# Optimization experiments

Hardware: AMD Instinct MI355X
Metric: run time of the kernel (lower is better)

## Reference

```python
import jax, jax.numpy as jnp
import numpy as np
from jax import lax

EPS = 1e-5      # BatchNorm eps
SLOPE = 0.01    # LeakyReLU negative slope
SHIFT = 0.5     # ShiftedLeakyReLU downward shift (assumed)

# sign with clipped straight-through estimator (hardtanh STE)
@jax.custom_vjp
def binarize(x):
    return jnp.sign(x)

def _bin_fwd(x):
    return jnp.sign(x), x

def _bin_bwd(res, g):
    x = res
    return (g * (jnp.abs(x) <= 1.0).astype(g.dtype),)

binarize.defvjp(_bin_fwd, _bin_bwd)


def conv2d(x, w, b, stride, padding, groups):
    # x: [B,Cin,H,W], w: [Cout,Cin//groups,kh,kw]
    y = lax.conv_general_dilated(
        x, w,
        window_strides=(stride, stride),
        padding=[(padding, padding), (padding, padding)],
        dimension_numbers=('NCHW', 'OIHW', 'NCHW'),
        feature_group_count=groups,
    )
    return y + b[None, :, None, None]


def batchnorm(x, gamma, beta):
    # training-mode BN: batch statistics over (N,H,W)
    mean = jnp.mean(x, axis=(0, 2, 3), keepdims=True)
    var = jnp.var(x, axis=(0, 2, 3), keepdims=True)
    xn = (x - mean) * lax.rsqrt(var + EPS)
    return xn * gamma[None, :, None, None] + beta[None, :, None, None]


def shifted_leaky_relu(x):
    return jax.nn.leaky_relu(x, SLOPE) - SHIFT


def block(x, w, b, gamma, beta, stride, padding, groups, binarize_w):
    wq = binarize(w) if binarize_w else w
    x = conv2d(x, wq, b, stride, padding, groups)
    x = batchnorm(x, gamma, beta)
    x = shifted_leaky_relu(x)
    return binarize(x)


def setup_inputs() -> dict:
    D, B, C, NCLS = 10000, 16, 1, 10
    key = jax.random.key(0)
    ks = jax.random.split(key, 6)
    u = lambda k, shape: jax.random.uniform(k, shape, jnp.float32, -1.0, 1.0)
    return {
        "x":  jax.random.normal(ks[0], (B, C, 28, 28), jnp.float32),
        "W1": u(ks[1], (D, C, 5, 5)),  "b1": jnp.zeros((D,), jnp.float32),
        "g1": jnp.ones((D,), jnp.float32), "be1": jnp.zeros((D,), jnp.float32),
        "W2": u(ks[2], (D, 1, 3, 3)),  "b2": jnp.zeros((D,), jnp.float32),
        "g2": jnp.ones((D,), jnp.float32), "be2": jnp.zeros((D,), jnp.float32),
        "W3": u(ks[3], (D, 1, 6, 6)) * 0.1, "b3": jnp.zeros((D,), jnp.float32),
        "g3": jnp.ones((D,), jnp.float32), "be3": jnp.zeros((D,), jnp.float32),
        "Wc": u(ks[4], (NCLS, D)),
    }


def reference(x, W1, b1, g1, be1, W2, b2, g2, be2, W3, b3, g3, be3, Wc):
    D = Wc.shape[1]
    # encoder: binary conv -> BN -> shifted leaky relu -> binarize
    h = block(x, W1, b1, g1, be1, stride=2, padding=1, groups=1, binarize_w=True)   # [B,D,13,13]
    h = block(h, W2, b2, g2, be2, stride=2, padding=0, groups=D, binarize_w=True)   # [B,D,6,6]
    # final prototype conv (plain fp32 weights, depthwise, collapses spatial dims)
    h = block(h, W3, b3, g3, be3, stride=1, padding=0, groups=D, binarize_w=False)  # [B,D,1,1]
    h = h.reshape(h.shape[0], -1)                                                   # [B,D]
    # centroid similarity with sign-binarized class hypervectors
    sims = h @ binarize(Wc).T                                                       # [B,n_classes]
    return sims / jnp.sqrt(jnp.float32(D))
```

## Files before the change

kernel.cpp:

```cpp
#include <hip/hip_runtime.h>
#include <stdint.h>

__device__ __forceinline__ float sgnf(float v) {
    return (v > 0.f) ? 1.f : ((v < 0.f) ? -1.f : 0.f);
}

__global__ void prep_w1(const float* __restrict__ W1, float* __restrict__ w1q) {
    const int i = blockIdx.x * 256 + threadIdx.x;
    if (i < 250000) w1q[i] = sgnf(W1[i]);
}

__global__ __launch_bounds__(256, 2) void hdc_fused(
    const float* __restrict__ x,  const float* __restrict__ w1q,
    const float* __restrict__ b1, const float* __restrict__ g1,
    const float* __restrict__ be1,
    const float* __restrict__ W2, const float* __restrict__ b2,
    const float* __restrict__ g2, const float* __restrict__ be2,
    const float* __restrict__ W3, const float* __restrict__ b3,
    const float* __restrict__ g3, const float* __restrict__ be3,
    const float* __restrict__ Wc, const float* __restrict__ zrow,
    float* __restrict__ out)
{
    __shared__ signed char h1s[8 * 2704];
    __shared__ float redbuf[2][4][8];
    __shared__ float h3buf[8 * 16];

    const int tid  = threadIdx.x;
    const int base = blockIdx.x * 8;

    const bool act = (tid < 208);
    const int oy = tid >> 4, bb = tid & 15;
    const int wv = tid >> 6, ln = tid & 63;

    for (int sg = 0; sg < 2; ++sg) {
        const int d0 = base + 4 * sg;
        const float* __restrict__ wp = w1q + d0 * 25;

        float acc[4][13];
        #pragma unroll
        for (int c = 0; c < 4; ++c) {
            const float bv = b1[d0 + c];
            #pragma unroll
            for (int i = 0; i < 13; ++i) acc[c][i] = bv;
        }

        if (act) {
            #pragma unroll
            for (int ky = 0; ky < 5; ++ky) {
                const int rr_ = 2 * oy - 1 + ky;
                const float* rp = (rr_ >= 0) ? (x + bb * 784 + rr_ * 28) : zrow;
                float r[29];
                r[0] = 0.f;
                #pragma unroll
                for (int j = 0; j < 7; ++j) {
                    float4 v = ((const float4*)rp)[j];
                    r[4 * j + 1] = v.x; r[4 * j + 2] = v.y;
                    r[4 * j + 3] = v.z; r[4 * j + 4] = v.w;
                }
                #pragma unroll
                for (int kx = 0; kx < 5; ++kx) {
                    #pragma unroll
                    for (int c = 0; c < 4; ++c) {
                        const float wk = wp[c * 25 + 5 * ky + kx];
                        #pragma unroll
                        for (int ox = 0; ox < 13; ++ox)
                            acc[c][ox] = fmaf(r[2 * ox + kx], wk, acc[c][ox]);
                    }
                }
            }
        }

        {
            float s[4] = {0.f, 0.f, 0.f, 0.f};
            if (act) {
                #pragma unroll
                for (int c = 0; c < 4; ++c)
                    #pragma unroll
                    for (int i = 0; i < 13; ++i) s[c] += acc[c][i];
            }
            #pragma unroll
            for (int m = 32; m >= 1; m >>= 1)
                #pragma unroll
                for (int c = 0; c < 4; ++c) s[c] += __shfl_xor(s[c], m, 64);
            if (ln == 0) {
                #pragma unroll
                for (int c = 0; c < 4; ++c) redbuf[sg][wv][c] = s[c];
            }
        }
        __syncthreads();
        float mu[4];
        #pragma unroll
        for (int c = 0; c < 4; ++c)
            mu[c] = (redbuf[sg][0][c] + redbuf[sg][1][c]
                   + redbuf[sg][2][c] + redbuf[sg][3][c]) / 2704.f;

        {
            float dv[4] = {0.f, 0.f, 0.f, 0.f};
            if (act) {
                #pragma unroll
                for (int c = 0; c < 4; ++c) {
                    #pragma unroll
                    for (int i = 0; i < 13; ++i) {
                        const float e = acc[c][i] - mu[c];
                        dv[c] = fmaf(e, e, dv[c]);
                    }
                }
            }
            #pragma unroll
            for (int m = 32; m >= 1; m >>= 1)
                #pragma unroll
                for (int c = 0; c < 4; ++c) dv[c] += __shfl_xor(dv[c], m, 64);
            if (ln == 0) {
                #pragma unroll
                for (int c = 0; c < 4; ++c) redbuf[sg][wv][4 + c] = dv[c];
            }
        }
        __syncthreads();

        float iv[4];
        #pragma unroll
        for (int c = 0; c < 4; ++c)
            iv[c] = rsqrtf((redbuf[sg][0][4 + c] + redbuf[sg][1][4 + c]
                          + redbuf[sg][2][4 + c] + redbuf[sg][3][4 + c]) / 2704.f + 1e-5f);
        if (act) {
            #pragma unroll
            for (int c = 0; c < 4; ++c) {
                const float ga = g1[d0 + c], bea = be1[d0 + c];
                signed char* hp = &h1s[(4 * sg + c) * 2704 + bb * 169 + oy * 13];
                #pragma unroll
                for (int i = 0; i < 13; ++i) {
                    const float xn = (acc[c][i] - mu[c]) * iv[c];
                    const float y  = fmaf(xn, ga, bea);
                    const float z  = ((y > 0.f) ? y : 0.01f * y) - 0.5f;
                    hp[i] = (z > 0.f) ? 1 : ((z < 0.f) ? -1 : 0);
                }
            }
        }
    }
    __syncthreads();

    if (tid < 128) {
        const int ch = tid >> 4, b_ = tid & 15;
        const int d = base + ch;
        float sw2[9];
        #pragma unroll
        for (int k = 0; k < 9; ++k) sw2[k] = sgnf(W2[d * 9 + k]);
        const float b2v = b2[d];
        const signed char* hp = &h1s[ch * 2704 + b_ * 169];

        float c2[36];
        #pragma unroll
        for (int oy2 = 0; oy2 < 6; ++oy2) {
            float rr[3][13];
            #pragma unroll
            for (int ky = 0; ky < 3; ++ky)
                #pragma unroll
                for (int j = 0; j < 13; ++j)
                    rr[ky][j] = (float)hp[(2 * oy2 + ky) * 13 + j];
            #pragma unroll
            for (int ox2 = 0; ox2 < 6; ++ox2) {
                float s = b2v;
                #pragma unroll
                for (int ky = 0; ky < 3; ++ky)
                    #pragma unroll
                    for (int kx = 0; kx < 3; ++kx)
                        s = fmaf(rr[ky][2 * ox2 + kx], sw2[3 * ky + kx], s);
                c2[oy2 * 6 + ox2] = s;
            }
        }

        float s2 = 0.f;
        #pragma unroll
        for (int i = 0; i < 36; ++i) s2 += c2[i];
        #pragma unroll
        for (int m = 8; m >= 1; m >>= 1) s2 += __shfl_xor(s2, m, 16);
        const float mu2 = s2 / 576.f;
        float d2 = 0.f;
        #pragma unroll
        for (int i = 0; i < 36; ++i) { const float e = c2[i] - mu2; d2 = fmaf(e, e, d2); }
        #pragma unroll
        for (int m = 8; m >= 1; m >>= 1) d2 += __shfl_xor(d2, m, 16);
        const float inv2 = rsqrtf(d2 / 576.f + 1e-5f);
        const float g2v = g2[d], be2v = be2[d];

        float z3 = b3[d];
        #pragma unroll
        for (int i = 0; i < 36; ++i) {
            const float xn = (c2[i] - mu2) * inv2;
            const float y  = fmaf(xn, g2v, be2v);
            const float z  = ((y > 0.f) ? y : 0.01f * y) - 0.5f;
            const float h2 = (z > 0.f) ? 1.f : ((z < 0.f) ? -1.f : 0.f);
            z3 = fmaf(h2, W3[d * 36 + i], z3);
        }

        float s3 = z3;
        #pragma unroll
        for (int m = 8; m >= 1; m >>= 1) s3 += __shfl_xor(s3, m, 16);
        const float mu3 = s3 / 16.f;
        const float e3 = z3 - mu3;
        float d3 = e3 * e3;
        #pragma unroll
        for (int m = 8; m >= 1; m >>= 1) d3 += __shfl_xor(d3, m, 16);
        const float inv3 = rsqrtf(d3 / 16.f + 1e-5f);
        const float xn3 = (z3 - mu3) * inv3;
        const float y3  = fmaf(xn3, g3[d], be3[d]);
        const float zz  = ((y3 > 0.f) ? y3 : 0.01f * y3) - 0.5f;
        h3buf[tid] = (zz > 0.f) ? 1.f : ((zz < 0.f) ? -1.f : 0.f);
    }
    __syncthreads();

    if (tid < 160) {
        const int bq = tid / 10, cq = tid - bq * 10;
        float ssum = 0.f;
        #pragma unroll
        for (int ch = 0; ch < 8; ++ch)
            ssum += h3buf[ch * 16 + bq] * sgnf(Wc[cq * 10000 + base + ch]);
        atomicAdd(&out[bq * 10 + cq], ssum);
    }
}

__global__ void hdc_scale(float* __restrict__ out) {
    const int i = threadIdx.x;
    if (i < 160) out[i] = out[i] / 100.0f;
}

extern "C" void kernel_launch(void* const* d_in, const int* in_sizes, int n_in,
                              void* d_out, int out_size, void* d_ws, size_t ws_size,
                              hipStream_t stream) {
    const float* x   = (const float*)d_in[0];
    const float* W1  = (const float*)d_in[1];
    const float* b1  = (const float*)d_in[2];
    const float* g1  = (const float*)d_in[3];
    const float* be1 = (const float*)d_in[4];
    const float* W2  = (const float*)d_in[5];
    const float* b2  = (const float*)d_in[6];
    const float* g2  = (const float*)d_in[7];
    const float* be2 = (const float*)d_in[8];
    const float* W3  = (const float*)d_in[9];
    const float* b3  = (const float*)d_in[10];
    const float* g3  = (const float*)d_in[11];
    const float* be3 = (const float*)d_in[12];
    const float* Wc  = (const float*)d_in[13];
    float* out  = (float*)d_out;
    float* w1q  = (float*)d_ws;
    float* zrow = (float*)d_ws + 250000;

    hipMemsetAsync(out, 0, 160 * sizeof(float), stream);
    hipMemsetAsync(zrow, 0, 128, stream);

    prep_w1<<<dim3(977), dim3(256), 0, stream>>>(W1, w1q);
    hdc_fused<<<dim3(1250), dim3(256), 0, stream>>>(
        x, w1q, b1, g1, be1, W2, b2, g2, be2, W3, b3, g3, be3, Wc, zrow, out);
    hdc_scale<<<dim3(1), dim3(192), 0, stream>>>(out);
}
```

Before: 79.61 us.

## Rebalance channel work into 1024 blocks and fold memsets and scale into kernels

The grid shrinks from 1250 to 1024 blocks: the first 452 blocks handle 12 channels and the rest handle 8, so the whole grid fits in one wave across the CUs. The two memsets are folded into prep_w1, and the separate scale kernel is dropped by dividing inside the atomicAdd. Wc signs are staged in shared memory by otherwise idle threads. The cost is more shared memory and a longer critical path for the heavy blocks.

After: 74.53 us. 6.4% less time.

```diff
diff --git a/kernel.cpp b/kernel.cpp
--- a/kernel.cpp
+++ b/kernel.cpp
@@ -5,9 +5,14 @@
     return (v > 0.f) ? 1.f : ((v < 0.f) ? -1.f : 0.f);
 }
 
-__global__ void prep_w1(const float* __restrict__ W1, float* __restrict__ w1q) {
+__global__ void prep_w1(const float* __restrict__ W1, float* __restrict__ w1q,
+                        float* __restrict__ out, float* __restrict__ zrow) {
     const int i = blockIdx.x * 256 + threadIdx.x;
     if (i < 250000) w1q[i] = sgnf(W1[i]);
+    if (blockIdx.x == 0) {
+        if (threadIdx.x < 160) out[threadIdx.x] = 0.f;
+        else if (threadIdx.x < 192) zrow[threadIdx.x - 160] = 0.f;
+    }
 }
 
 __global__ __launch_bounds__(256, 2) void hdc_fused(
@@ -21,18 +26,22 @@
     const float* __restrict__ Wc, const float* __restrict__ zrow,
     float* __restrict__ out)
 {
-    __shared__ signed char h1s[8 * 2704];
-    __shared__ float redbuf[2][4][8];
-    __shared__ float h3buf[8 * 16];
-
-    const int tid  = threadIdx.x;
-    const int base = blockIdx.x * 8;
+    __shared__ signed char h1s[12 * 2704];
+    __shared__ float redbuf[3][4][8];
+    __shared__ float h3buf[12 * 16];
+    __shared__ float wcs[120];
+
+    const int tid = threadIdx.x;
+    const bool heavy = (blockIdx.x < 452);
+    const int nch  = heavy ? 12 : 8;
+    const int nsw  = heavy ? 3 : 2;
+    const int base = heavy ? blockIdx.x * 12 : 5424 + (blockIdx.x - 452) * 8;
 
     const bool act = (tid < 208);
     const int oy = tid >> 4, bb = tid & 15;
     const int wv = tid >> 6, ln = tid & 63;
 
-    for (int sg = 0; sg < 2; ++sg) {
+    for (int sg = 0; sg < nsw; ++sg) {
         const int d0 = base + 4 * sg;
         const float* __restrict__ wp = w1q + d0 * 25;
 
@@ -139,7 +148,7 @@
     }
     __syncthreads();
 
-    if (tid < 128) {
+    if (tid < 16 * nch) {
         const int ch = tid >> 4, b_ = tid & 15;
         const int d = base + ch;
         float sw2[9];
@@ -206,22 +215,19 @@
         const float y3  = fmaf(xn3, g3[d], be3[d]);
         const float zz  = ((y3 > 0.f) ? y3 : 0.01f * y3) - 0.5f;
         h3buf[tid] = (zz > 0.f) ? 1.f : ((zz < 0.f) ? -1.f : 0.f);
+    } else if (tid >= 192) {
+        for (int i = tid - 192; i < 10 * nch; i += 64)
+            wcs[i] = sgnf(Wc[(i % 10) * 10000 + base + (i / 10)]);
     }
     __syncthreads();
 
     if (tid < 160) {
         const int bq = tid / 10, cq = tid - bq * 10;
         float ssum = 0.f;
-        #pragma unroll
-        for (int ch = 0; ch < 8; ++ch)
-            ssum += h3buf[ch * 16 + bq] * sgnf(Wc[cq * 10000 + base + ch]);
-        atomicAdd(&out[bq * 10 + cq], ssum);
-    }
-}
-
-__global__ void hdc_scale(float* __restrict__ out) {
-    const int i = threadIdx.x;
-    if (i < 160) out[i] = out[i] / 100.0f;
+        for (int ch = 0; ch < nch; ++ch)
+            ssum += h3buf[ch * 16 + bq] * wcs[ch * 10 + cq];
+        atomicAdd(&out[bq * 10 + cq], ssum / 100.0f);
+    }
 }
 
 extern "C" void kernel_launch(void* const* d_in, const int* in_sizes, int n_in,
@@ -245,11 +251,7 @@
     float* w1q  = (float*)d_ws;
     float* zrow = (float*)d_ws + 250000;
 
-    hipMemsetAsync(out, 0, 160 * sizeof(float), stream);
-    hipMemsetAsync(zrow, 0, 128, stream);
-
-    prep_w1<<<dim3(977), dim3(256), 0, stream>>>(W1, w1q);
-    hdc_fused<<<dim3(1250), dim3(256), 0, stream>>>(
+    prep_w1<<<dim3(977), dim3(256), 0, stream>>>(W1, w1q, out, zrow);
+    hdc_fused<<<dim3(1024), dim3(256), 0, stream>>>(
         x, w1q, b1, g1, be1, W2, b2, g2, be2, W3, b3, g3, be3, Wc, zrow, out);
-    hdc_scale<<<dim3(1), dim3(192), 0, stream>>>(out);
-}
+}
```
